# Performance work log

Measured on AMD Instinct MI355X. Metric: run time of the kernel, lower is better.

Reference implementation:

```python
import jax, jax.numpy as jnp
import numpy as np

U = 50  # lstm units

def lstm_seq(x, Wx, Wh, b):
    # x: [B,S,D] -> h: [B,S,U], Keras LSTMCell gate order i,f,g,o
    B = x.shape[0]
    xz = jnp.einsum('bsd,dk->bsk', x, Wx) + b  # [B,S,4U]
    def step(carry, zt):
        h, c = carry
        z = zt + h @ Wh
        i, f, g, o = jnp.split(z, 4, axis=-1)
        c = jax.nn.sigmoid(f) * c + jax.nn.sigmoid(i) * jnp.tanh(g)
        h = jax.nn.sigmoid(o) * jnp.tanh(c)
        return (h, c), h
    init = (jnp.zeros((B, U), x.dtype), jnp.zeros((B, U), x.dtype))
    _, hs = jax.lax.scan(step, init, jnp.swapaxes(xz, 0, 1))
    return jnp.swapaxes(hs, 0, 1)

def bilstm(x, fWx, fWh, fb, bWx, bWh, bb):
    # Keras RNN(go_backwards=True) does NOT re-reverse outputs; concat as-is.
    fw = lstm_seq(x, fWx, fWh, fb)
    bw = lstm_seq(x[:, ::-1, :], bWx, bWh, bb)
    return jnp.concatenate([fw, bw], axis=-1)

def local_inference(x1e, m1, x2e, m2):
    # Literal translation: inputs are batch-first [B,S,D]; the TF code transposes
    # to [S,B,D] and batch-matmuls over the leading (seq) axis, so attention is
    # over the batch index at each timestep. A[s,i,j] = x1e[i,s]. x2e[j,s]
    A = jnp.einsum('isd,jsd->sij', x1e, x2e)
    m1t = m1.T  # [S,B]
    m2t = m2.T
    w2 = jnp.exp(A - jnp.max(A, axis=2, keepdims=True)) * m2t[:, None, :]
    alpha = w2 / (jnp.sum(w2, axis=-1, keepdims=True) + 1e-8)
    x1_dual = jnp.einsum('sij,jsd->isd', alpha, x2e)  # [B,S,D]
    A1 = A - jnp.max(A, axis=1, keepdims=True)
    w1 = jnp.exp(jnp.swapaxes(A1, 1, 2)) * m1t[:, None, :]
    beta = w1 / (jnp.sum(w1, axis=-1, keepdims=True) + 1e-8)
    x2_dual = jnp.einsum('sji,isd->jsd', beta, x1e)  # [B,S,D]
    return x1_dual, x2_dual

def esim_forward(x1, x2, emb, b1f_Wx, b1f_Wh, b1f_b, b1b_Wx, b1b_Wh, b1b_b,
                 dense_W, dense_b, b2f_Wx, b2f_Wh, b2f_b, b2b_Wx, b2b_Wh, b2b_b,
                 dense1_W, dense1_b, out_W, out_b):
    m1 = (x1 != 0).astype(jnp.float32)
    m2 = (x2 != 0).astype(jnp.float32)
    e1 = emb[x1] * m1[..., None]
    e2 = emb[x2] * m2[..., None]
    enc1 = bilstm(e1, b1f_Wx, b1f_Wh, b1f_b, b1b_Wx, b1b_Wh, b1b_b) * m1[..., None]
    enc2 = bilstm(e2, b1f_Wx, b1f_Wh, b1f_b, b1b_Wx, b1b_Wh, b1b_b) * m2[..., None]
    d1, d2 = local_inference(enc1, m1, enc2, m2)
    match1 = jnp.concatenate([enc1, d1, enc1 * d1, enc1 - d1], axis=2)
    match2 = jnp.concatenate([enc2, d2, enc2 * d2, enc2 - d2], axis=2)
    map1 = jax.nn.relu(match1 @ dense_W + dense_b)
    map2 = jax.nn.relu(match2 @ dense_W + dense_b)
    cmp1 = bilstm(map1, b2f_Wx, b2f_Wh, b2f_b, b2b_Wx, b2b_Wh, b2b_b)
    cmp2 = bilstm(map2, b2f_Wx, b2f_Wh, b2f_b, b2b_Wx, b2b_Wh, b2b_b)
    c1m = cmp1 * m1[..., None]
    c2m = cmp2 * m2[..., None]
    p1_sum = jnp.sum(c1m, axis=1) / jnp.sum(m1, axis=1)[:, None]
    p1_max = jnp.max(c1m, axis=1)
    p2_sum = jnp.sum(c2m, axis=1) / jnp.sum(m2, axis=1)[:, None]
    p2_max = jnp.max(c2m, axis=1)
    logit = jnp.concatenate([p1_sum, p1_max, p2_sum, p2_max], axis=1)
    logit = jnp.tanh(logit @ dense1_W + dense1_b)
    logit = logit @ out_W + out_b
    return jax.nn.softmax(logit, axis=-1)

def setup_inputs() -> dict:
    key = jax.random.key(0)
    ks = jax.random.split(key, 24)
    B, S, V, E = 128, 512, 20000, 50
    def w(k, shape, s=0.05):
        return jax.random.normal(k, shape, dtype=jnp.float32) * s
    return {
        'x1': jax.random.randint(ks[0], (B, S), 0, V, dtype=jnp.int32),
        'x2': jax.random.randint(ks[1], (B, S), 0, V, dtype=jnp.int32),
        'emb': jax.random.uniform(ks[2], (V, E), jnp.float32, -0.05, 0.05),
        'b1f_Wx': w(ks[3], (E, 4 * U)), 'b1f_Wh': w(ks[4], (U, 4 * U)), 'b1f_b': w(ks[5], (4 * U,)),
        'b1b_Wx': w(ks[6], (E, 4 * U)), 'b1b_Wh': w(ks[7], (U, 4 * U)), 'b1b_b': w(ks[8], (4 * U,)),
        'dense_W': w(ks[9], (400, 100), 0.02), 'dense_b': jnp.zeros((100,), jnp.float32),
        'b2f_Wx': w(ks[10], (100, 4 * U)), 'b2f_Wh': w(ks[11], (U, 4 * U)), 'b2f_b': w(ks[12], (4 * U,)),
        'b2b_Wx': w(ks[13], (100, 4 * U)), 'b2b_Wh': w(ks[14], (U, 4 * U)), 'b2b_b': w(ks[15], (4 * U,)),
        'dense1_W': w(ks[16], (400, 100), 0.02), 'dense1_b': jnp.zeros((100,), jnp.float32),
        'out_W': w(ks[17], (100, 2), 0.02), 'out_b': jnp.zeros((2,), jnp.float32),
    }

def reference(x1, x2, emb, b1f_Wx, b1f_Wh, b1f_b, b1b_Wx, b1b_Wh, b1b_b,
              dense_W, dense_b, b2f_Wx, b2f_Wh, b2f_b, b2b_Wx, b2b_Wh, b2b_b,
              dense1_W, dense1_b, out_W, out_b):
    return esim_forward(x1, x2, emb, b1f_Wx, b1f_Wh, b1f_b, b1b_Wx, b1b_Wh, b1b_b,
                        dense_W, dense_b, b2f_Wx, b2f_Wh, b2f_b, b2b_Wx, b2b_Wh, b2b_b,
                        dense1_W, dense1_b, out_W, out_b)
```

## Files before the change

kernel.cpp:

```cpp
#include <hip/hip_runtime.h>

#define TOKN 65536
#define SQ 512
#define BB 128
#define DD 100
#define APAD 132

typedef unsigned short bf16t;
typedef __attribute__((ext_vector_type(8))) short bf16x8;
typedef __attribute__((ext_vector_type(4))) float floatx4;
typedef __attribute__((ext_vector_type(2))) _Float16 half2t;

__device__ __forceinline__ float bf2f(bf16t v) {
  unsigned u = ((unsigned)v) << 16;
  return __uint_as_float(u);
}
__device__ __forceinline__ bf16t f2bf(float x) {
  unsigned u = __float_as_uint(x);
  unsigned r = u + 0x7FFFu + ((u >> 16) & 1u);
  return (bf16t)(r >> 16);
}
__device__ __forceinline__ float2 ldpair(const float* p) { return *(const float2*)p; }
__device__ __forceinline__ float2 ldpair(const bf16t* p) {
  unsigned u = *(const unsigned*)p;
  float2 r;
  r.x = __uint_as_float(u << 16);
  r.y = __uint_as_float(u & 0xFFFF0000u);
  return r;
}
__device__ __forceinline__ half2t u2h2(unsigned u) {
  union { unsigned u; half2t h; } x; x.u = u; return x.h;
}

__device__ __forceinline__ float sigm(float x) { return 1.f / (1.f + __expf(-x)); }
__device__ __forceinline__ float tanhx(float x) { return 1.f - 2.f / (1.f + __expf(2.f * x)); }

#if __has_builtin(__builtin_amdgcn_fdot2)
#define DOT2(hu, wu, acc) acc = __builtin_amdgcn_fdot2(u2h2(hu), u2h2(wu), acc, false);
#else
#define DOT2(hu, wu, acc) { half2t hh = u2h2(hu), ww = u2h2(wu); \
  acc = fmaf((float)hh[0], (float)ww[0], acc); \
  acc = fmaf((float)hh[1], (float)ww[1], acc); }
#endif

__global__ __launch_bounds__(256) void embed_kernel(
    const int* __restrict__ x1, const int* __restrict__ x2,
    const float* __restrict__ emb,
    bf16t* __restrict__ e1, bf16t* __restrict__ e2,
    float* __restrict__ m1, float* __restrict__ m2) {
  const int which = blockIdx.y;
  const int* __restrict__ x = which ? x2 : x1;
  bf16t* __restrict__ e = which ? e2 : e1;
  float* __restrict__ m = which ? m2 : m1;
  int idx = blockIdx.x * 256 + threadIdx.x;
  int t = idx >> 6, d = idx & 63;
  int tok = x[t];
  float mk = (tok != 0) ? 1.f : 0.f;
  float v = (d < 50) ? emb[tok * 50 + d] * mk : 0.f;
  e[idx] = f2bf(v);
  if (d == 0) m[t] = mk;
}

__global__ __launch_bounds__(256) void padzero_kernel(
    unsigned* __restrict__ p1, unsigned* __restrict__ p2) {
  int idx = blockIdx.x * 256 + threadIdx.x;
  if (idx >= TOKN * 14) return;
  int t = idx / 14, d = idx - t * 14;
  p1[(size_t)t * 64 + 50 + d] = 0u;
  p2[(size_t)t * 64 + 50 + d] = 0u;
}

__global__ __launch_bounds__(256) void wprep_kernel(
    const float* __restrict__ w1f, const float* __restrict__ w1b,
    const float* __restrict__ w2f, const float* __restrict__ w2b,
    const float* __restrict__ dW,
    const float* __restrict__ h1f, const float* __restrict__ h1b,
    const float* __restrict__ h2f, const float* __restrict__ h2b,
    bf16t* __restrict__ w1T, bf16t* __restrict__ w2T, bf16t* __restrict__ wdT,
    unsigned* __restrict__ whP) {
  int idx = blockIdx.x * 256 + threadIdx.x;
  int sec = blockIdx.y;
  if (sec == 0) {
    if (idx >= 2 * 208 * 64) return;
    int d = idx / (208 * 64), r = idx % (208 * 64);
    int n = r >> 6, k = r & 63;
    const float* W = d ? w1b : w1f;
    float v = (n < 200 && k < 50) ? W[k * 200 + n] : 0.f;
    w1T[idx] = f2bf(v);
  } else if (sec == 1) {
    if (idx >= 2 * 208 * 128) return;
    int d = idx / (208 * 128), r = idx % (208 * 128);
    int n = r >> 7, k = r & 127;
    const float* W = d ? w2b : w2f;
    float v = (n < 200 && k < 100) ? W[k * 200 + n] : 0.f;
    w2T[idx] = f2bf(v);
  } else if (sec == 2) {
    if (idx >= 128 * 384) return;
    int n = idx / 384, kv = idx % 384;
    int reg = kv >> 7, kk = kv & 127;
    float v = 0.f;
    if (n < 100 && kk < 100) {
      if (reg == 0) v = dW[kk * 100 + n] + dW[(300 + kk) * 100 + n];
      else if (reg == 1) v = dW[(100 + kk) * 100 + n] - dW[(300 + kk) * 100 + n];
      else v = dW[(200 + kk) * 100 + n];
    }
    wdT[idx] = f2bf(v);
  } else {
    if (idx >= 4 * 25 * 200) return;
    int sd = idx / 5000, r = idx % 5000;
    int k2 = r / 200, colx = r % 200;
    const float* W = (sd == 0) ? h1f : (sd == 1) ? h1b : (sd == 2) ? h2f : h2b;
    float v0 = W[(2 * k2) * 200 + colx];
    float v1 = W[(2 * k2 + 1) * 200 + colx];
    union { _Float16 h[2]; unsigned u; } p;
    p.h[0] = (_Float16)v0;
    p.h[1] = (_Float16)v1;
    whP[idx] = p.u;
  }
}

template <int KP>
__global__ __launch_bounds__(256) void xz_mfma(
    const bf16t* __restrict__ A1, const bf16t* __restrict__ A2,
    const bf16t* __restrict__ WT,
    const float* __restrict__ bf_, const float* __restrict__ bb_,
    bf16t* __restrict__ out) {
  const int combo = blockIdx.y;
  const bf16t* __restrict__ A = (combo < 2) ? A1 : A2;
  const bf16t* __restrict__ W = WT + (size_t)(combo & 1) * 208 * KP;
  const float* __restrict__ bias = (combo & 1) ? bb_ : bf_;
  bf16t* __restrict__ O = out + (size_t)combo * TOKN * 200;
  const int tid = threadIdx.x;
  const int wave = tid >> 6, lane = tid & 63;
  const int m0 = blockIdx.x * 64 + wave * 16;
  const int l15 = lane & 15, quad = lane >> 4;
  floatx4 acc[13];
#pragma unroll
  for (int nt = 0; nt < 13; ++nt) acc[nt] = (floatx4){0.f, 0.f, 0.f, 0.f};
  const bf16t* __restrict__ arow = A + (size_t)(m0 + l15) * KP + quad * 8;
  const bf16t* __restrict__ wb = W + (size_t)l15 * KP + quad * 8;
#pragma unroll
  for (int ks = 0; ks < KP / 32; ++ks) {
    bf16x8 a = *(const bf16x8*)(arow + ks * 32);
#pragma unroll
    for (int nt = 0; nt < 13; ++nt) {
      bf16x8 b = *(const bf16x8*)(wb + (size_t)nt * 16 * KP + ks * 32);
      acc[nt] = __builtin_amdgcn_mfma_f32_16x16x32_bf16(a, b, acc[nt], 0, 0, 0);
    }
  }
  const int crow = m0 + quad * 4;
  const int bidx = crow >> 9;
  const int trow = crow & 511;
#pragma unroll
  for (int nt = 0; nt < 13; ++nt) {
    int n = nt * 16 + l15;
    if (n < 200) {
      float bn = bias[n];
      union { bf16t h[4]; uint2 u2; } pk;
#pragma unroll
      for (int r = 0; r < 4; ++r) pk.h[r] = f2bf(acc[nt][r] + bn);
      *(uint2*)&O[((size_t)bidx * 200 + n) * SQ + trow] = pk.u2;
    }
  }
}

__global__ __launch_bounds__(256) void dense_mfma(
    const bf16t* __restrict__ enc1, const bf16t* __restrict__ enc2,
    const bf16t* __restrict__ d1b, const bf16t* __restrict__ d2b,
    const bf16t* __restrict__ wdT, const float* __restrict__ bias,
    bf16t* __restrict__ map1, bf16t* __restrict__ map2) {
  const int inp = blockIdx.y;
  const bf16t* __restrict__ E = inp ? enc2 : enc1;
  const bf16t* __restrict__ Db = inp ? d2b : d1b;
  bf16t* __restrict__ O = inp ? map2 : map1;
  const int tid = threadIdx.x;
  const int wave = tid >> 6, lane = tid & 63;
  const int m0 = blockIdx.x * 64 + wave * 16;
  const int l15 = lane & 15, quad = lane >> 4;
  floatx4 acc[8];
#pragma unroll
  for (int nt = 0; nt < 8; ++nt) acc[nt] = (floatx4){0.f, 0.f, 0.f, 0.f};
  const bf16t* __restrict__ erow = E + (size_t)(m0 + l15) * 128 + quad * 8;
  const bf16t* __restrict__ drow = Db + (size_t)(m0 + l15) * 128 + quad * 8;
  const bf16t* __restrict__ wb = wdT + (size_t)l15 * 384 + quad * 8;
#pragma unroll
  for (int ks = 0; ks < 4; ++ks) {
    bf16x8 ae = *(const bf16x8*)(erow + ks * 32);
    bf16x8 ad = *(const bf16x8*)(drow + ks * 32);
    bf16x8 aed;
#pragma unroll
    for (int q = 0; q < 8; ++q) {
      float pe = bf2f((bf16t)ae[q]);
      float pd = bf2f((bf16t)ad[q]);
      aed[q] = (short)f2bf(pe * pd);
    }
#pragma unroll
    for (int nt = 0; nt < 8; ++nt) {
      const bf16t* wn = wb + (size_t)nt * 16 * 384 + ks * 32;
      bf16x8 b0 = *(const bf16x8*)(wn);
      acc[nt] = __builtin_amdgcn_mfma_f32_16x16x32_bf16(ae, b0, acc[nt], 0, 0, 0);
      bf16x8 b1 = *(const bf16x8*)(wn + 128);
      acc[nt] = __builtin_amdgcn_mfma_f32_16x16x32_bf16(ad, b1, acc[nt], 0, 0, 0);
      bf16x8 b2 = *(const bf16x8*)(wn + 256);
      acc[nt] = __builtin_amdgcn_mfma_f32_16x16x32_bf16(aed, b2, acc[nt], 0, 0, 0);
    }
  }
  const int crow = m0 + quad * 4;
#pragma unroll
  for (int nt = 0; nt < 8; ++nt) {
    int n = nt * 16 + l15;
    float bn = (n < 100) ? bias[n] : 0.f;
#pragma unroll
    for (int r = 0; r < 4; ++r) {
      float v = (n < 100) ? fmaxf(acc[nt][r] + bn, 0.f) : 0.f;
      O[(size_t)(crow + r) * 128 + n] = f2bf(v);
    }
  }
}

#define WLIST(X) X(0) X(1) X(2) X(3) X(4) X(5) X(6) X(7) X(8) X(9) X(10) X(11) \
  X(12) X(13) X(14) X(15) X(16) X(17) X(18) X(19) X(20) X(21) X(22) X(23) X(24)
#define WDECL(i) unsigned w##i = wsrc[i * 200 + colc];
#define WPIN(i) asm volatile("" : "+v"(w##i));

__global__ __launch_bounds__(256)
__attribute__((amdgpu_waves_per_eu(2, 2)))
void lstm_scan(
    const bf16t* __restrict__ xzT,
    const unsigned* __restrict__ whPL,
    bf16t* __restrict__ out1, bf16t* __restrict__ out2,
    const float* __restrict__ m1, const float* __restrict__ m2,
    int hasMask) {
  const int blk = blockIdx.x;
  const int scan = blk >> 7;
  const int b = blk & 127;
  const int inp = scan >> 1;
  const int dir = scan & 1;
  const int tid = threadIdx.x;
  const int lane = tid & 63;
  const int u = tid >> 2, g = tid & 3;
  const int col = g * 50 + u;
  const bool active = (tid < 200);
  const int colc = active ? col : 0;
  const bf16t* __restrict__ xcol =
      xzT + (((size_t)scan * 128 + b) * 200 + colc) * SQ;
  bf16t* __restrict__ outp = (inp ? out2 : out1) + (size_t)b * SQ * 128 + dir * 50;
  const float* __restrict__ mk = (inp ? m2 : m1) + b * SQ;
  __shared__ __align__(16) unsigned hbuf[2][32];

  const unsigned* __restrict__ wsrc = whPL + dir * 5000;
  WLIST(WDECL)
  WLIST(WPIN)

  if (tid < 64) ((unsigned*)hbuf)[tid] = 0;
  float c = 0.f;
  const bool msk = hasMask && active && (g == 0);
  const float4* mk4 = (const float4*)mk;

  uint4 zcur, znxt;
  {
    int r0 = dir ? (SQ - 8) : 0;
    int r1 = dir ? (SQ - 16) : 8;
    zcur = *(const uint4*)(xcol + r0);
    znxt = *(const uint4*)(xcol + r1);
  }
  __syncthreads();

  for (int g8 = 0; g8 < SQ / 8; ++g8) {
    float zf[8];
    {
      unsigned d0 = zcur.x, d1 = zcur.y, d2 = zcur.z, d3 = zcur.w;
      zf[0] = __uint_as_float(d0 << 16);
      zf[1] = __uint_as_float(d0 & 0xFFFF0000u);
      zf[2] = __uint_as_float(d1 << 16);
      zf[3] = __uint_as_float(d1 & 0xFFFF0000u);
      zf[4] = __uint_as_float(d2 << 16);
      zf[5] = __uint_as_float(d2 & 0xFFFF0000u);
      zf[6] = __uint_as_float(d3 << 16);
      zf[7] = __uint_as_float(d3 & 0xFFFF0000u);
    }
    uint4 zfol = znxt;
    {
      int gnext = (g8 + 2 < SQ / 8) ? (g8 + 2) : (SQ / 8 - 1);
      int rn = dir ? (SQ - 8 - 8 * gnext) : (8 * gnext);
      znxt = *(const uint4*)(xcol + rn);
    }
    float mva[8];
    if (msk) {
      float4 ma = mk4[2 * g8], mb = mk4[2 * g8 + 1];
      mva[0] = ma.x; mva[1] = ma.y; mva[2] = ma.z; mva[3] = ma.w;
      mva[4] = mb.x; mva[5] = mb.y; mva[6] = mb.z; mva[7] = mb.w;
    }
    bf16t hsave[8];
#pragma unroll
    for (int j = 0; j < 8; ++j) {
      const int par = j & 1;
      float z0v = dir ? zf[7 - j] : zf[j];
      const uint4* hp = (const uint4*)&hbuf[par][0];
      uint4 q0 = hp[0], q1 = hp[1], q2 = hp[2], q3 = hp[3], q4 = hp[4], q5 = hp[5];
      unsigned qL = hbuf[par][24];
      float za = z0v, zb = 0.f, zc = 0.f, zd = 0.f;
      DOT2(q0.x, w0, za)  DOT2(q0.y, w1, zb)
      DOT2(q0.z, w2, zc)  DOT2(q0.w, w3, zd)
      DOT2(q1.x, w4, za)  DOT2(q1.y, w5, zb)
      DOT2(q1.z, w6, zc)  DOT2(q1.w, w7, zd)
      DOT2(q2.x, w8, za)  DOT2(q2.y, w9, zb)
      DOT2(q2.z, w10, zc) DOT2(q2.w, w11, zd)
      DOT2(q3.x, w12, za) DOT2(q3.y, w13, zb)
      DOT2(q3.z, w14, zc) DOT2(q3.w, w15, zd)
      DOT2(q4.x, w16, za) DOT2(q4.y, w17, zb)
      DOT2(q4.z, w18, zc) DOT2(q4.w, w19, zd)
      DOT2(q5.x, w20, za) DOT2(q5.y, w21, zb)
      DOT2(q5.z, w22, zc) DOT2(q5.w, w23, zd)
      DOT2(qL,   w24, za)
      float zv = (za + zb) + (zc + zd);
      float a = (g == 2) ? tanhx(zv) : sigm(zv);
      int base = lane & ~3;
      float af = __shfl(a, base + 1);
      float ag_ = __shfl(a, base + 2);
      float ao = __shfl(a, base + 3);
      if (active && g == 0) {
        c = af * c + a * ag_;
        float hn = ao * tanhx(c);
        ((_Float16*)&hbuf[par ^ 1][0])[u] = (_Float16)hn;
        float mv = hasMask ? mva[j] : 1.f;
        hsave[j] = f2bf(hn * mv);
      }
      __syncthreads();
    }
    if (active && g == 0) {
      int t0 = 8 * g8;
#pragma unroll
      for (int j = 0; j < 8; ++j)
        outp[(size_t)(t0 + j) * 128 + u] = hsave[j];
    }
    zcur = zfol;
  }
}

__global__ __launch_bounds__(256) void attn_kernel(
    const bf16t* __restrict__ enc1, const bf16t* __restrict__ enc2,
    const float* __restrict__ m1, const float* __restrict__ m2,
    bf16t* __restrict__ d1b, bf16t* __restrict__ d2b) {
  const int s = blockIdx.x;
  const int tid = threadIdx.x;
  __shared__ __align__(16) float E1[BB][DD];
  __shared__ __align__(16) float E2[BB + 1][DD];
  __shared__ __align__(16) float Ah[64][APAD];
  __shared__ float mk1[BB], mk2[BB];
  __shared__ float rden[64];

  for (int idx = tid; idx < BB * 50; idx += 256) {
    int i = idx / 50, dp = idx - i * 50;
    float2 v1 = ldpair(enc1 + ((size_t)i * SQ + s) * 128 + 2 * dp);
    E1[i][2 * dp] = v1.x;
    E1[i][2 * dp + 1] = v1.y;
    float2 v2 = ldpair(enc2 + ((size_t)i * SQ + s) * 128 + 2 * dp);
    E2[i][2 * dp] = v2.x;
    E2[i][2 * dp + 1] = v2.y;
  }
  if (tid < BB) {
    mk1[tid] = m1[tid * SQ + s];
    mk2[tid] = m2[tid * SQ + s];
  }
  __syncthreads();

  const int ti = tid >> 4, tjj = tid & 15;
  const int xj = tid & 127;
  const int xd0 = (tid >> 7) * 50;
  float N[50];
#pragma unroll
  for (int q = 0; q < 50; ++q) N[q] = 0.f;
  float Dacc = 0.f, M = -1e30f;

  for (int half = 0; half < 2; ++half) {
    const int r0 = half * 64;
    float acc[4][8];
#pragma unroll
    for (int ii = 0; ii < 4; ++ii)
#pragma unroll
      for (int jj = 0; jj < 8; ++jj) acc[ii][jj] = 0.f;
    for (int k = 0; k < DD; k += 4) {
      float4 a4[4], b4[8];
#pragma unroll
      for (int ii = 0; ii < 4; ++ii)
        a4[ii] = *(const float4*)&E1[r0 + 4 * ti + ii][k];
#pragma unroll
      for (int jj = 0; jj < 8; ++jj)
        b4[jj] = *(const float4*)&E2[tjj + 16 * jj][k];
#pragma unroll
      for (int ii = 0; ii < 4; ++ii)
#pragma unroll
        for (int jj = 0; jj < 8; ++jj)
          acc[ii][jj] += a4[ii].x * b4[jj].x + a4[ii].y * b4[jj].y +
                         a4[ii].z * b4[jj].z + a4[ii].w * b4[jj].w;
    }
#pragma unroll
    for (int ii = 0; ii < 4; ++ii)
#pragma unroll
      for (int jj = 0; jj < 8; ++jj)
        Ah[4 * ti + ii][tjj + 16 * jj] = acc[ii][jj];
    __syncthreads();

    {
      float lm = M;
      for (int i = 0; i < 64; ++i) lm = fmaxf(lm, Ah[i][xj]);
      float scale = __expf(M - lm);
      Dacc *= scale;
#pragma unroll
      for (int q = 0; q < 50; ++q) N[q] *= scale;
      for (int i = 0; i < 64; ++i) {
        float p = __expf(Ah[i][xj] - lm) * mk1[r0 + i];
        Dacc += p;
        const float2* e1p = (const float2*)&E1[r0 + i][xd0];
#pragma unroll
        for (int q = 0; q < 25; ++q) {
          float2 ev = e1p[q];
          N[2 * q] += p * ev.x;
          N[2 * q + 1] += p * ev.y;
        }
      }
      M = lm;
    }
    __syncthreads();

    {
      int row = tid >> 2, seg = tid & 3;
      float mx = -1e30f;
      for (int q = 0; q < 32; ++q) mx = fmaxf(mx, Ah[row][seg + 4 * q]);
      mx = fmaxf(mx, __shfl_xor(mx, 1));
      mx = fmaxf(mx, __shfl_xor(mx, 2));
      float sm = 0.f;
      for (int q = 0; q < 32; ++q) {
        int jc = seg + 4 * q;
        float p = __expf(Ah[row][jc] - mx) * mk2[jc];
        Ah[row][jc] = p;
        sm += p;
      }
      sm += __shfl_xor(sm, 1);
      sm += __shfl_xor(sm, 2);
      if (seg == 0) rden[row] = sm + 1e-8f;
    }
    __syncthreads();

    {
      float o[4][8];
#pragma unroll
      for (int ii = 0; ii < 4; ++ii)
#pragma unroll
        for (int jj = 0; jj < 8; ++jj) o[ii][jj] = 0.f;
      for (int jb = 0; jb < BB; ++jb) {
        float pv[4], ev[8];
#pragma unroll
        for (int ii = 0; ii < 4; ++ii) pv[ii] = Ah[4 * ti + ii][jb];
#pragma unroll
        for (int jj = 0; jj < 8; ++jj) ev[jj] = E2[jb][tjj + 16 * jj];
#pragma unroll
        for (int ii = 0; ii < 4; ++ii)
#pragma unroll
          for (int jj = 0; jj < 8; ++jj) o[ii][jj] += pv[ii] * ev[jj];
      }
#pragma unroll
      for (int ii = 0; ii < 4; ++ii) {
        int i = r0 + 4 * ti + ii;
        float inv = 1.f / rden[4 * ti + ii];
#pragma unroll
        for (int jj = 0; jj < 8; ++jj) {
          int d = tjj + 16 * jj;
          float val = (d < DD) ? o[ii][jj] * inv : 0.f;
          d1b[((size_t)i * SQ + s) * 128 + d] = f2bf(val);
        }
      }
    }
    __syncthreads();
  }
  float invD = 1.f / (Dacc + 1e-8f);
#pragma unroll
  for (int q = 0; q < 50; ++q)
    d2b[((size_t)xj * SQ + s) * 128 + xd0 + q] = f2bf(N[q] * invD);
  if (xd0 == 50) {
#pragma unroll
    for (int q = 0; q < 28; ++q)
      d2b[((size_t)xj * SQ + s) * 128 + 100 + q] = 0;
  }
}

__global__ __launch_bounds__(128) void pool_kernel(
    const bf16t* __restrict__ cmp1, const bf16t* __restrict__ cmp2,
    const float* __restrict__ m1, const float* __restrict__ m2,
    float* __restrict__ pooled) {
  int b = blockIdx.x & 127, inp = blockIdx.x >> 7;
  const bf16t* C = (inp ? cmp2 : cmp1) + (size_t)b * SQ * 128;
  const float* M = (inp ? m2 : m1) + b * SQ;
  int f = threadIdx.x;
  float ms = 0.f;
  for (int s = f; s < SQ; s += 128) ms += M[s];
  __shared__ float red[128];
  red[f] = ms;
  __syncthreads();
  for (int o = 64; o > 0; o >>= 1) {
    if (f < o) red[f] += red[f + o];
    __syncthreads();
  }
  float msum = red[0];
  if (f < 100) {
    float sm = 0.f, mx = -1e30f;
    for (int s = 0; s < SQ; ++s) {
      float v = bf2f(C[(size_t)s * 128 + f]) * M[s];
      sm += v;
      mx = fmaxf(mx, v);
    }
    pooled[b * 400 + inp * 200 + f] = sm / msum;
    pooled[b * 400 + inp * 200 + 100 + f] = mx;
  }
}

__global__ __launch_bounds__(128) void final_kernel(
    const float* __restrict__ pooled, const float* __restrict__ W1,
    const float* __restrict__ b1, const float* __restrict__ W2,
    const float* __restrict__ b2, float* __restrict__ out) {
  int b = blockIdx.x;
  int j = threadIdx.x;
  __shared__ float pr[400];
  __shared__ float h[100];
  for (int idx = j; idx < 400; idx += 128) pr[idx] = pooled[b * 400 + idx];
  __syncthreads();
  if (j < 100) {
    float a = b1[j];
    for (int k = 0; k < 400; ++k) a += pr[k] * W1[k * 100 + j];
    h[j] = tanhx(a);
  }
  __syncthreads();
  if (j == 0) {
    float l0 = b2[0], l1 = b2[1];
    for (int k = 0; k < 100; ++k) {
      l0 += h[k] * W2[k * 2];
      l1 += h[k] * W2[k * 2 + 1];
    }
    float mx = fmaxf(l0, l1);
    float e0 = __expf(l0 - mx), e1 = __expf(l1 - mx);
    float inv = 1.f / (e0 + e1);
    out[b * 2] = e0 * inv;
    out[b * 2 + 1] = e1 * inv;
  }
}

extern "C" void kernel_launch(void* const* d_in, const int* in_sizes, int n_in,
                              void* d_out, int out_size, void* d_ws, size_t ws_size,
                              hipStream_t stream) {
  const int* x1 = (const int*)d_in[0];
  const int* x2 = (const int*)d_in[1];
  const float* emb = (const float*)d_in[2];
  const float* b1f_Wx = (const float*)d_in[3];
  const float* b1f_Wh = (const float*)d_in[4];
  const float* b1f_b = (const float*)d_in[5];
  const float* b1b_Wx = (const float*)d_in[6];
  const float* b1b_Wh = (const float*)d_in[7];
  const float* b1b_b = (const float*)d_in[8];
  const float* dense_W = (const float*)d_in[9];
  const float* dense_b = (const float*)d_in[10];
  const float* b2f_Wx = (const float*)d_in[11];
  const float* b2f_Wh = (const float*)d_in[12];
  const float* b2f_b = (const float*)d_in[13];
  const float* b2b_Wx = (const float*)d_in[14];
  const float* b2b_Wh = (const float*)d_in[15];
  const float* b2b_b = (const float*)d_in[16];
  const float* dense1_W = (const float*)d_in[17];
  const float* dense1_b = (const float*)d_in[18];
  const float* out_W = (const float*)d_in[19];
  const float* out_b = (const float*)d_in[20];
  float* out = (float*)d_out;

  char* base = (char*)d_ws;
  bf16t* xz = (bf16t*)base;
  bf16t* d1b = (bf16t*)base;
  bf16t* d2b = d1b + (size_t)TOKN * 128;
  char* r1 = base + (size_t)4 * TOKN * 200 * 2;
  bf16t* enc1 = (bf16t*)r1;
  bf16t* enc2 = enc1 + (size_t)TOKN * 128;
  bf16t* e1b = (bf16t*)r1;
  bf16t* e2b = e1b + (size_t)TOKN * 64;
  char* r2 = r1 + (size_t)2 * TOKN * 128 * 2;
  bf16t* map1 = (bf16t*)r2;
  bf16t* map2 = map1 + (size_t)TOKN * 128;
  char* r3 = r2 + (size_t)2 * TOKN * 128 * 2;
  float* m1 = (float*)r3;
  float* m2 = m1 + TOKN;
  float* pooled = m2 + TOKN;
  bf16t* w1T = (bf16t*)(r3 + ((size_t)2 * TOKN + 128 * 400) * 4);
  bf16t* w2T = w1T + 2 * 208 * 64;
  bf16t* wdT = w2T + 2 * 208 * 128;
  unsigned* whP = (unsigned*)(wdT + 128 * 384);
  bf16t* cmp1 = enc1;
  bf16t* cmp2 = enc2;
  (void)in_sizes; (void)n_in; (void)out_size; (void)ws_size;

  embed_kernel<<<dim3(TOKN * 64 / 256, 2), 256, 0, stream>>>(
      x1, x2, emb, e1b, e2b, m1, m2);
  wprep_kernel<<<dim3(208, 4), 256, 0, stream>>>(
      b1f_Wx, b1b_Wx, b2f_Wx, b2b_Wx, dense_W,
      b1f_Wh, b1b_Wh, b2f_Wh, b2b_Wh, w1T, w2T, wdT, whP);
  xz_mfma<64><<<dim3(TOKN / 64, 4), 256, 0, stream>>>(
      e1b, e2b, w1T, b1f_b, b1b_b, xz);
  padzero_kernel<<<(TOKN * 14 + 255) / 256, 256, 0, stream>>>(
      (unsigned*)enc1, (unsigned*)enc2);
  lstm_scan<<<512, 256, 0, stream>>>(xz, whP, enc1, enc2, m1, m2, 1);
  attn_kernel<<<SQ, 256, 0, stream>>>(enc1, enc2, m1, m2, d1b, d2b);
  dense_mfma<<<dim3(TOKN / 64, 2), 256, 0, stream>>>(
      enc1, enc2, d1b, d2b, wdT, dense_b, map1, map2);
  xz_mfma<128><<<dim3(TOKN / 64, 4), 256, 0, stream>>>(
      map1, map2, w2T, b2f_b, b2b_b, xz);
  lstm_scan<<<512, 256, 0, stream>>>(xz, whP + 2 * 5000, cmp1, cmp2, m1, m2, 0);
  pool_kernel<<<256, 128, 0, stream>>>(cmp1, cmp2, m1, m2, pooled);
  final_kernel<<<128, 128, 0, stream>>>(pooled, dense1_W, dense1_b, out_W, out_b, out);
}
```

Before: 1.139 ms.

## Run LSTM scan in a single wave with all four gates per lane

The recurrent scan kernel moves from 256 threads (one thread per gate column, combined through shuffles and a block barrier each step) to 64 threads, where each lane owns one hidden unit and computes all four gates. Each lane now keeps 100 recurrent-weight registers and streams four input-projection columns. This removes the per-timestep __syncthreads and the cross-lane shuffles, which were the main cost on the serial critical path. In exchange, each lane does four times the dot-product work per step, register pressure rises, and occupancy is lower.

```diff
diff --git a/kernel.cpp b/kernel.cpp
--- a/kernel.cpp
+++ b/kernel.cpp
@@ -218,13 +218,8 @@
   }
 }
 
-#define WLIST(X) X(0) X(1) X(2) X(3) X(4) X(5) X(6) X(7) X(8) X(9) X(10) X(11) \
-  X(12) X(13) X(14) X(15) X(16) X(17) X(18) X(19) X(20) X(21) X(22) X(23) X(24)
-#define WDECL(i) unsigned w##i = wsrc[i * 200 + colc];
-#define WPIN(i) asm volatile("" : "+v"(w##i));
-
-__global__ __launch_bounds__(256)
-__attribute__((amdgpu_waves_per_eu(2, 2)))
+__global__ __launch_bounds__(64)
+__attribute__((amdgpu_waves_per_eu(1, 2)))
 void lstm_scan(
     const bf16t* __restrict__ xzT,
     const unsigned* __restrict__ whPL,
@@ -236,105 +231,117 @@
   const int b = blk & 127;
   const int inp = scan >> 1;
   const int dir = scan & 1;
-  const int tid = threadIdx.x;
-  const int lane = tid & 63;
-  const int u = tid >> 2, g = tid & 3;
-  const int col = g * 50 + u;
-  const bool active = (tid < 200);
-  const int colc = active ? col : 0;
-  const bf16t* __restrict__ xcol =
-      xzT + (((size_t)scan * 128 + b) * 200 + colc) * SQ;
+  const int u = threadIdx.x;
+  const bool act_l = (u < 50);
+  const int uc = act_l ? u : 0;
+  const bf16t* __restrict__ xbase = xzT + ((size_t)scan * 128 + b) * 200 * SQ;
+  const bf16t* __restrict__ xi = xbase + (size_t)uc * SQ;
+  const bf16t* __restrict__ xf = xbase + (size_t)(50 + uc) * SQ;
+  const bf16t* __restrict__ xg = xbase + (size_t)(100 + uc) * SQ;
+  const bf16t* __restrict__ xo = xbase + (size_t)(150 + uc) * SQ;
   bf16t* __restrict__ outp = (inp ? out2 : out1) + (size_t)b * SQ * 128 + dir * 50;
   const float* __restrict__ mk = (inp ? m2 : m1) + b * SQ;
   __shared__ __align__(16) unsigned hbuf[2][32];
 
   const unsigned* __restrict__ wsrc = whPL + dir * 5000;
-  WLIST(WDECL)
-  WLIST(WPIN)
-
-  if (tid < 64) ((unsigned*)hbuf)[tid] = 0;
+  unsigned wgt[4][25];
+#pragma unroll
+  for (int gg = 0; gg < 4; ++gg)
+#pragma unroll
+    for (int k2 = 0; k2 < 25; ++k2)
+      wgt[gg][k2] = wsrc[k2 * 200 + gg * 50 + uc];
+#pragma unroll
+  for (int gg = 0; gg < 4; ++gg)
+#pragma unroll
+    for (int k2 = 0; k2 < 25; ++k2)
+      asm volatile("" : "+v"(wgt[gg][k2]));
+
+  ((unsigned*)hbuf)[u] = 0;
   float c = 0.f;
-  const bool msk = hasMask && active && (g == 0);
   const float4* mk4 = (const float4*)mk;
 
-  uint4 zcur, znxt;
+  uint4 zc0, zc1, zc2, zc3, zn0, zn1, zn2, zn3;
   {
     int r0 = dir ? (SQ - 8) : 0;
     int r1 = dir ? (SQ - 16) : 8;
-    zcur = *(const uint4*)(xcol + r0);
-    znxt = *(const uint4*)(xcol + r1);
-  }
-  __syncthreads();
+    zc0 = *(const uint4*)(xi + r0); zn0 = *(const uint4*)(xi + r1);
+    zc1 = *(const uint4*)(xf + r0); zn1 = *(const uint4*)(xf + r1);
+    zc2 = *(const uint4*)(xg + r0); zn2 = *(const uint4*)(xg + r1);
+    zc3 = *(const uint4*)(xo + r0); zn3 = *(const uint4*)(xo + r1);
+  }
 
   for (int g8 = 0; g8 < SQ / 8; ++g8) {
-    float zf[8];
+    float zst[4][8];
     {
-      unsigned d0 = zcur.x, d1 = zcur.y, d2 = zcur.z, d3 = zcur.w;
-      zf[0] = __uint_as_float(d0 << 16);
-      zf[1] = __uint_as_float(d0 & 0xFFFF0000u);
-      zf[2] = __uint_as_float(d1 << 16);
-      zf[3] = __uint_as_float(d1 & 0xFFFF0000u);
-      zf[4] = __uint_as_float(d2 << 16);
-      zf[5] = __uint_as_float(d2 & 0xFFFF0000u);
-      zf[6] = __uint_as_float(d3 << 16);
-      zf[7] = __uint_as_float(d3 & 0xFFFF0000u);
-    }
-    uint4 zfol = znxt;
+      uint4 cur[4] = {zc0, zc1, zc2, zc3};
+#pragma unroll
+      for (int gg = 0; gg < 4; ++gg) {
+        unsigned dw[4] = {cur[gg].x, cur[gg].y, cur[gg].z, cur[gg].w};
+#pragma unroll
+        for (int p = 0; p < 4; ++p) {
+          float lo = __uint_as_float(dw[p] << 16);
+          float hi = __uint_as_float(dw[p] & 0xFFFF0000u);
+          if (dir) { zst[gg][7 - 2 * p] = lo; zst[gg][6 - 2 * p] = hi; }
+          else     { zst[gg][2 * p] = lo;     zst[gg][2 * p + 1] = hi; }
+        }
+      }
+    }
+    uint4 zf0 = zn0, zf1 = zn1, zf2 = zn2, zf3 = zn3;
     {
       int gnext = (g8 + 2 < SQ / 8) ? (g8 + 2) : (SQ / 8 - 1);
       int rn = dir ? (SQ - 8 - 8 * gnext) : (8 * gnext);
-      znxt = *(const uint4*)(xcol + rn);
+      zn0 = *(const uint4*)(xi + rn);
+      zn1 = *(const uint4*)(xf + rn);
+      zn2 = *(const uint4*)(xg + rn);
+      zn3 = *(const uint4*)(xo + rn);
     }
     float mva[8];
-    if (msk) {
+    if (hasMask) {
       float4 ma = mk4[2 * g8], mb = mk4[2 * g8 + 1];
       mva[0] = ma.x; mva[1] = ma.y; mva[2] = ma.z; mva[3] = ma.w;
       mva[4] = mb.x; mva[5] = mb.y; mva[6] = mb.z; mva[7] = mb.w;
     }
-    bf16t hsave[8];
+    bf16t hs8[8];
 #pragma unroll
     for (int j = 0; j < 8; ++j) {
       const int par = j & 1;
-      float z0v = dir ? zf[7 - j] : zf[j];
       const uint4* hp = (const uint4*)&hbuf[par][0];
       uint4 q0 = hp[0], q1 = hp[1], q2 = hp[2], q3 = hp[3], q4 = hp[4], q5 = hp[5];
       unsigned qL = hbuf[par][24];
-      float za = z0v, zb = 0.f, zc = 0.f, zd = 0.f;
-      DOT2(q0.x, w0, za)  DOT2(q0.y, w1, zb)
-      DOT2(q0.z, w2, zc)  DOT2(q0.w, w3, zd)
-      DOT2(q1.x, w4, za)  DOT2(q1.y, w5, zb)
-      DOT2(q1.z, w6, zc)  DOT2(q1.w, w7, zd)
-      DOT2(q2.x, w8, za)  DOT2(q2.y, w9, zb)
-      DOT2(q2.z, w10, zc) DOT2(q2.w, w11, zd)
-      DOT2(q3.x, w12, za) DOT2(q3.y, w13, zb)
-      DOT2(q3.z, w14, zc) DOT2(q3.w, w15, zd)
-      DOT2(q4.x, w16, za) DOT2(q4.y, w17, zb)
-      DOT2(q4.z, w18, zc) DOT2(q4.w, w19, zd)
-      DOT2(q5.x, w20, za) DOT2(q5.y, w21, zb)
-      DOT2(q5.z, w22, zc) DOT2(q5.w, w23, zd)
-      DOT2(qL,   w24, za)
-      float zv = (za + zb) + (zc + zd);
-      float a = (g == 2) ? tanhx(zv) : sigm(zv);
-      int base = lane & ~3;
-      float af = __shfl(a, base + 1);
-      float ag_ = __shfl(a, base + 2);
-      float ao = __shfl(a, base + 3);
-      if (active && g == 0) {
-        c = af * c + a * ag_;
-        float hn = ao * tanhx(c);
+      unsigned hd[25] = {q0.x, q0.y, q0.z, q0.w, q1.x, q1.y, q1.z, q1.w,
+                         q2.x, q2.y, q2.z, q2.w, q3.x, q3.y, q3.z, q3.w,
+                         q4.x, q4.y, q4.z, q4.w, q5.x, q5.y, q5.z, q5.w, qL};
+      float res[4];
+#pragma unroll
+      for (int gg = 0; gg < 4; ++gg) {
+        float a0 = zst[gg][j], a1 = 0.f;
+#pragma unroll
+        for (int k2 = 0; k2 < 24; k2 += 2) {
+          DOT2(hd[k2], wgt[gg][k2], a0)
+          DOT2(hd[k2 + 1], wgt[gg][k2 + 1], a1)
+        }
+        DOT2(hd[24], wgt[gg][24], a0)
+        res[gg] = a0 + a1;
+      }
+      float ai = sigm(res[0]);
+      float af = sigm(res[1]);
+      float ag = tanhx(res[2]);
+      float ao = sigm(res[3]);
+      c = af * c + ai * ag;
+      float hn = ao * tanhx(c);
+      if (act_l) {
         ((_Float16*)&hbuf[par ^ 1][0])[u] = (_Float16)hn;
         float mv = hasMask ? mva[j] : 1.f;
-        hsave[j] = f2bf(hn * mv);
+        hs8[j] = f2bf(hn * mv);
       }
-      __syncthreads();
-    }
-    if (active && g == 0) {
+    }
+    if (act_l) {
       int t0 = 8 * g8;
 #pragma unroll
       for (int j = 0; j < 8; ++j)
-        outp[(size_t)(t0 + j) * 128 + u] = hsave[j];
-    }
-    zcur = zfol;
+        outp[(size_t)(t0 + j) * 128 + u] = hs8[j];
+    }
+    zc0 = zf0; zc1 = zf1; zc2 = zf2; zc3 = zf3;
   }
 }
 
@@ -604,13 +611,13 @@
       e1b, e2b, w1T, b1f_b, b1b_b, xz);
   padzero_kernel<<<(TOKN * 14 + 255) / 256, 256, 0, stream>>>(
       (unsigned*)enc1, (unsigned*)enc2);
-  lstm_scan<<<512, 256, 0, stream>>>(xz, whP, enc1, enc2, m1, m2, 1);
+  lstm_scan<<<512, 64, 0, stream>>>(xz, whP, enc1, enc2, m1, m2, 1);
   attn_kernel<<<SQ, 256, 0, stream>>>(enc1, enc2, m1, m2, d1b, d2b);
   dense_mfma<<<dim3(TOKN / 64, 2), 256, 0, stream>>>(
       enc1, enc2, d1b, d2b, wdT, dense_b, map1, map2);
   xz_mfma<128><<<dim3(TOKN / 64, 4), 256, 0, stream>>>(
       map1, map2, w2T, b2f_b, b2b_b, xz);
-  lstm_scan<<<512, 256, 0, stream>>>(xz, whP + 2 * 5000, cmp1, cmp2, m1, m2, 0);
+  lstm_scan<<<512, 64, 0, stream>>>(xz, whP + 2 * 5000, cmp1, cmp2, m1, m2, 0);
   pool_kernel<<<256, 128, 0, stream>>>(cmp1, cmp2, m1, m2, pooled);
   final_kernel<<<128, 128, 0, stream>>>(pooled, dense1_W, dense1_b, out_W, out_b, out);
 }
```

New measurement: 1.055 ms. -7.4%, faster.
